# Kernel tuning notes

Measured on AMD Instinct MI355X. Metric: run time of the kernel, lower is better.

The kernel has to match this reference:

```python
import jax, jax.numpy as jnp
import numpy as np

DEPTH_BINS = 39
FEAT = 64
IMG_H, IMG_W = 448, 800
DS = 16
HF, WF = IMG_H // DS, IMG_W // DS  # 28, 50
D_MIN, D_MAX = 2.0, 80.0
BEV_X0 = 0.0
BEV_Y0 = -50.4
RES = 0.8
HB, WB = 188, 126
BN_EPS = 1e-5


def make_frustum():
    # (D, Hf, Wf, 3) points (u*d, v*d, d) at receptive-field centers
    step = (D_MAX - D_MIN) / DEPTH_BINS
    depths = jnp.linspace(D_MIN + step / 2, D_MAX - step / 2, DEPTH_BINS)
    u = jnp.arange(WF, dtype=jnp.float32) * DS + DS / 2
    v = jnp.arange(HF, dtype=jnp.float32) * DS + DS / 2
    d = jnp.broadcast_to(depths[:, None, None], (DEPTH_BINS, HF, WF))
    ug = jnp.broadcast_to(u[None, None, :], (DEPTH_BINS, HF, WF))
    vg = jnp.broadcast_to(v[None, :, None], (DEPTH_BINS, HF, WF))
    return jnp.stack([ug * d, vg * d, d], axis=-1)


def conv2d(x, w, b):
    y = jax.lax.conv_general_dilated(x, w, (1, 1), 'SAME', dimension_numbers=('NCHW', 'OIHW', 'NCHW'))
    return y + b[None, :, None, None]


def bn(x, g, b, m, v):
    s = (g * jax.lax.rsqrt(v + BN_EPS))[None, :, None, None]
    return (x - m[None, :, None, None]) * s + b[None, :, None, None]


def lss_forward(head, intrinsics, car2cams, w1, b1, g1, be1, m1, v1, w2, b2, g2, be2, m2, v2, w3, b3, g3, be3, m3, v3, w4, b4):
    B, N = intrinsics.shape[:2]
    # CamEncoder head: depth softmax x feature outer product (lift)
    depth = jax.nn.softmax(head[:, :DEPTH_BINS], axis=1)       # (BN, D, Hf, Wf)
    feat = head[:, DEPTH_BINS:]                                # (BN, C, Hf, Wf)
    vol = depth[:, :, None] * feat[:, None]                    # (BN, D, C, Hf, Wf)
    vol = vol.reshape(B, N, DEPTH_BINS, FEAT, HF, WF).transpose(0, 1, 2, 4, 5, 3)  # (B,N,D,Hf,Wf,C)
    # get_geometry: frustum -> car frame
    frustum = make_frustum()
    frust_h = jnp.concatenate([frustum, jnp.ones((DEPTH_BINS, HF, WF, 1), jnp.float32)], axis=-1)
    inv_K3 = jnp.linalg.inv(intrinsics)
    inv_K = jnp.zeros((B, N, 4, 4), jnp.float32).at[..., :3, :3].set(inv_K3).at[..., 3, 3].set(1.0)
    T = jnp.linalg.inv(car2cams) @ inv_K                       # (B,N,4,4)
    geom = jnp.einsum('bnij,dhwj->bndhwi', T, frust_h)[..., :3]  # (B,N,D,Hf,Wf,3)
    # voxel_pool: masked scatter-add into BEV grid (int cast truncates toward 0, matching torch .long())
    bx = ((geom[..., 0] - BEV_X0) / RES).astype(jnp.int32)
    by = ((geom[..., 1] - BEV_Y0) / RES).astype(jnp.int32)
    mask = (bx >= 0) & (bx < HB) & (by >= 0) & (by < WB)
    M = N * DEPTH_BINS * HF * WF
    feat_flat = (vol * mask[..., None]).reshape(B * M, FEAT)
    idx = jnp.where(mask, bx * WB + by, 0).reshape(B, M)
    idx = (idx + jnp.arange(B)[:, None] * (HB * WB)).reshape(-1)
    bev = jax.ops.segment_sum(feat_flat, idx, num_segments=B * HB * WB)
    bev = bev.reshape(B, HB, WB, FEAT).transpose(0, 3, 1, 2)   # (B,C,HB,WB)
    # BEVDecoder (eval-mode BN)
    x = jax.nn.relu(bn(conv2d(bev, w1, b1), g1, be1, m1, v1))
    x = jax.nn.relu(bn(conv2d(x, w2, b2), g2, be2, m2, v2))
    x = jax.nn.relu(bn(conv2d(x, w3, b3), g3, be3, m3, v3))
    return conv2d(x, w4, b4)                                   # (B,1,HB,WB)


def setup_inputs() -> dict:
    key = jax.random.key(0)
    ks = jax.random.split(key, 8)
    B, N = 2, 6
    head = jax.random.normal(ks[0], (B * N, DEPTH_BINS + FEAT, HF, WF), dtype=jnp.float32)
    # realistic invertible intrinsics
    f = 500.0 + 25.0 * jax.random.normal(ks[1], (B, N))
    K = (jnp.zeros((B, N, 3, 3))
         .at[..., 0, 0].set(f).at[..., 1, 1].set(f)
         .at[..., 0, 2].set(IMG_W / 2).at[..., 1, 2].set(IMG_H / 2)
         .at[..., 2, 2].set(1.0)).astype(jnp.float32)
    # cam->car rotation: car X = cam z (forward), car Y = -cam x, car Z = -cam y (up)
    R = jnp.array([[0.0, 0.0, 1.0], [-1.0, 0.0, 0.0], [0.0, -1.0, 0.0]], jnp.float32)
    t = jnp.array([2.0, 0.0, 1.3], jnp.float32) + 0.3 * jax.random.normal(ks[2], (B, N, 3))
    cam2car = (jnp.zeros((B, N, 4, 4))
               .at[..., :3, :3].set(R).at[..., :3, 3].set(t).at[..., 3, 3].set(1.0))
    car2cams = jnp.linalg.inv(cam2car).astype(jnp.float32)

    def w(k, shape, fan_in):
        return jax.random.normal(k, shape, dtype=jnp.float32) * (1.0 / np.sqrt(fan_in))

    inp = dict(head=head, intrinsics=K, car2cams=car2cams)
    inp.update(w1=w(ks[3], (128, FEAT, 3, 3), FEAT * 9), b1=jnp.zeros(128), g1=jnp.ones(128), be1=jnp.zeros(128), m1=jnp.zeros(128), v1=jnp.ones(128))
    inp.update(w2=w(ks[4], (128, 128, 3, 3), 128 * 9), b2=jnp.zeros(128), g2=jnp.ones(128), be2=jnp.zeros(128), m2=jnp.zeros(128), v2=jnp.ones(128))
    inp.update(w3=w(ks[5], (64, 128, 3, 3), 128 * 9), b3=jnp.zeros(64), g3=jnp.ones(64), be3=jnp.zeros(64), m3=jnp.zeros(64), v3=jnp.ones(64))
    inp.update(w4=w(ks[6], (1, 64, 1, 1), 64), b4=jnp.zeros(1))
    return inp


def reference(head, intrinsics, car2cams, w1, b1, g1, be1, m1, v1, w2, b2, g2, be2, m2, v2, w3, b3, g3, be3, m3, v3, w4, b4):
    return lss_forward(head, intrinsics, car2cams, w1, b1, g1, be1, m1, v1, w2, b2, g2, be2, m2, v2, w3, b3, g3, be3, m3, v3, w4, b4)
```

## Files before the change

kernel.cpp:

```cpp
#include <hip/hip_runtime.h>
#include <hip/hip_bf16.h>
#include <math.h>

#define NDEPTH 39
#define NFEAT 64
#define HF 28
#define WF 50
#define NPIXCAM (HF*WF)
#define HB 188
#define WB 126
#define NB (HB*WB)
#define BATCH 2
#define NCAM 12
#define NPIX (BATCH*NB)
#define NCELL NPIX
#define CH_IN (NDEPTH+NFEAT)
#define NPT (NCAM*NPIXCAM)
#define NPD (NPT*NDEPTH)
#define CPAD 16
#define SCAN_NB ((NCELL + 255) / 256)

typedef short bf16x8 __attribute__((ext_vector_type(8)));
typedef float f32x4 __attribute__((ext_vector_type(4)));

#define OFF_DIAG 0u
#define OFF_T    64u
#define OFF_B1   1024u
#define OFF_B2   1536u
#define OFF_B3   2048u
#define OFF_WP1  4096u
#define OFF_WP2  151552u
#define OFF_WP3  446464u
#define OFF_XIN  593920u
#define OFF_X1   6658048u
#define OFF_X2   18786304u
#define OFF_PROBS 30914560u
#define OFF_FEATT 33535360u
#define OFF_CUR   35685760u
#define OFF_START 38717824u
#define OFF_BSUM  38907392u
#define OFF_REC   38908416u
#define WS_NEEDED 44150016u

__device__ inline float bfraw2f(unsigned short u) {
  union { unsigned int i; float f; } c; c.i = ((unsigned int)u) << 16; return c.f;
}
__device__ inline float ldf(const void* p, size_t i, int mode) {
  if (mode == 0) return ((const float*)p)[i];
  if (mode == 1) return bfraw2f(((const unsigned short*)p)[i]);
  return (float)(((const _Float16*)p)[i]);
}

__global__ __launch_bounds__(256) void canary_kernel(float* out, int n, float val) {
  int i = blockIdx.x * 256 + threadIdx.x;
  if (i < n) out[i] = val;
}
__global__ __launch_bounds__(256) void probe_kernel(float* out, int n) {
  int i = blockIdx.x * 256 + threadIdx.x;
  if (i < n) out[i] = 16.0f;
}
__global__ void detect_mode_kernel(const void* g1, int* diag) {
  if (threadIdx.x == 0) {
    unsigned int bits = *(const unsigned int*)g1;
    int m = -1;
    if (bits == 0x3F800000u) m = 0;
    else if (bits == 0x3F803F80u) m = 1;
    else if (bits == 0x3C003C00u) m = 2;
    diag[0] = m;
  }
}

__global__ __launch_bounds__(64) void compute_T_kernel(
    const void* __restrict__ K, const void* __restrict__ C,
    const int* __restrict__ diag, float* __restrict__ T) {
  int i = threadIdx.x;
  if (i >= NCAM) return;
  int md = diag[0];
  if (md < 0) return;
  double a = ldf(K, i*9+0, md), b = ldf(K, i*9+1, md), c = ldf(K, i*9+2, md),
         d = ldf(K, i*9+3, md), e = ldf(K, i*9+4, md), f = ldf(K, i*9+5, md),
         g = ldf(K, i*9+6, md), h = ldf(K, i*9+7, md), ii = ldf(K, i*9+8, md);
  double det = a * (e * ii - f * h) - b * (d * ii - f * g) + c * (d * h - e * g);
  double id = 1.0 / det;
  double iK[4][4] = {
      {(e * ii - f * h) * id, (c * h - b * ii) * id, (b * f - c * e) * id, 0.0},
      {(f * g - d * ii) * id, (a * ii - c * g) * id, (c * d - a * f) * id, 0.0},
      {(d * h - e * g) * id, (b * g - a * h) * id, (a * e - b * d) * id, 0.0},
      {0.0, 0.0, 0.0, 1.0}};
  double M[4][8];
  for (int r = 0; r < 4; ++r)
    for (int cc = 0; cc < 4; ++cc) {
      M[r][cc] = ldf(C, (size_t)i * 16 + r * 4 + cc, md);
      M[r][cc + 4] = (r == cc) ? 1.0 : 0.0;
    }
  for (int col = 0; col < 4; ++col) {
    int piv = col;
    double pv = fabs(M[col][col]);
    for (int r = col + 1; r < 4; ++r) {
      double v = fabs(M[r][col]);
      if (v > pv) { pv = v; piv = r; }
    }
    if (piv != col)
      for (int cc = 0; cc < 8; ++cc) {
        double t = M[col][cc]; M[col][cc] = M[piv][cc]; M[piv][cc] = t;
      }
    double inv = 1.0 / M[col][col];
    for (int cc = 0; cc < 8; ++cc) M[col][cc] *= inv;
    for (int r = 0; r < 4; ++r)
      if (r != col) {
        double fa = M[r][col];
        for (int cc = 0; cc < 8; ++cc) M[r][cc] -= fa * M[col][cc];
      }
  }
  for (int r = 0; r < 4; ++r)
    for (int cc = 0; cc < 4; ++cc) {
      double sv = 0.0;
      for (int j = 0; j < 4; ++j) sv += M[r][4 + j] * iK[j][cc];
      T[i * 16 + r * 4 + cc] = (float)sv;
    }
}

__global__ void check_T_kernel(const float* __restrict__ T, int* diag) {
  if (threadIdx.x != 0 || blockIdx.x != 0) return;
  int bad = 0;
  for (int i = 0; i < NCAM * 16; ++i) {
    float x = T[i];
    if (!isfinite(x) || fabsf(x) > 1e7f) bad = 1;
  }
  for (int c = 0; c < NCAM; ++c)
    if (fabsf(T[c * 16 + 15] - 1.0f) > 0.01f) bad = 1;
  if (bad) diag[1] = 1;
}

template <int CIN, int COUT>
__global__ __launch_bounds__(256) void pack_kernel(
    const void* __restrict__ w, const void* __restrict__ bconv,
    const void* __restrict__ g, const void* __restrict__ be,
    const void* __restrict__ m, const void* __restrict__ v,
    const int* __restrict__ diag, __hip_bfloat16* __restrict__ wp,
    float* __restrict__ bias) {
  int md = diag[0];
  if (md < 0) return;
  int t = blockIdx.x * 256 + threadIdx.x;
  if (t < COUT) {
    float s = ldf(g, t, md) * (1.0f / sqrtf(ldf(v, t, md) + 1e-5f));
    bias[t] = (ldf(bconv, t, md) - ldf(m, t, md)) * s + ldf(be, t, md);
  }
  if (t >= 9 * CIN * COUT) return;
  constexpr int NOCB = COUT / 16, NICB = CIN / 32;
  int j = t & 7;
  int l = (t >> 3) & 63;
  int tile = t >> 9;
  int ocb = tile % NOCB;
  int rest = tile / NOCB;
  int icb = rest % NICB;
  int kykx = rest / NICB;
  int ic = icb * 32 + (l >> 4) * 8 + j;
  int oc = ocb * 16 + (l & 15);
  int ky = kykx / 3, kx = kykx - ky * 3;
  float s = ldf(g, oc, md) * (1.0f / sqrtf(ldf(v, oc, md) + 1e-5f));
  float wv = ldf(w, ((size_t)(oc * CIN + ic) * 3 + ky) * 3 + kx, md) * s;
  wp[t] = __float2bfloat16(wv);
}

__device__ inline int point_cell(const float* __restrict__ T, int cam, int rem, int d) {
  int h = rem / WF;
  int w = rem - h * WF;
  const float* Tm = T + cam * 16;
  float u = w * 16.0f + 8.0f;
  float v = h * 16.0f + 8.0f;
  float dep = 3.0f + 2.0f * d;
  float ud = u * dep, vd = v * dep;
  float gx = Tm[0] * ud + Tm[1] * vd + Tm[2] * dep + Tm[3];
  float gy = Tm[4] * ud + Tm[5] * vd + Tm[6] * dep + Tm[7];
  int bx = (int)((gx - 0.0f) / 0.8f);
  int by = (int)((gy - (-50.4f)) / 0.8f);
  if (bx >= 0 && bx < HB && by >= 0 && by < WB) {
    int b = cam / 6;
    return b * NB + bx * WB + by;
  }
  return -1;
}

__global__ __launch_bounds__(64) void prep_kernel2(
    const void* __restrict__ head, const float* __restrict__ T,
    const int* __restrict__ diag, float* __restrict__ probs,
    __hip_bfloat16* __restrict__ featT, int* __restrict__ curpad) {
  int md = diag[0];
  if (md < 0) return;
  int pix = blockIdx.x;
  int cam = pix / NPIXCAM;
  int rem = pix - cam * NPIXCAM;
  int lane = threadIdx.x;
  size_t base = (size_t)cam * CH_IN * NPIXCAM;

  float logit = (lane < NDEPTH) ? ldf(head, base + (size_t)lane * NPIXCAM + rem, md)
                                : -INFINITY;
  float mx = logit;
  for (int o = 32; o; o >>= 1) mx = fmaxf(mx, __shfl_xor(mx, o, 64));
  float e = (lane < NDEPTH) ? expf(logit - mx) : 0.0f;
  float s = e;
  for (int o = 32; o; o >>= 1) s += __shfl_xor(s, o, 64);
  if (lane < NDEPTH) probs[(size_t)pix * NDEPTH + lane] = e / s;

  float feat = ldf(head, base + (size_t)(NDEPTH + lane) * NPIXCAM + rem, md);
  featT[(size_t)pix * NFEAT + lane] = __float2bfloat16(feat);

  if (lane < NDEPTH) {
    int cell = point_cell(T, cam, rem, lane);
    if (cell >= 0) atomicAdd(&curpad[cell * CPAD], 1);
  }
}

__global__ __launch_bounds__(256) void scan_phase1(
    const int* __restrict__ curpad, int* __restrict__ start,
    int* __restrict__ bsum) {
  int cell = blockIdx.x * 256 + threadIdx.x;
  int c = (cell < NCELL) ? curpad[cell * CPAD] : 0;
  __shared__ int sh[256];
  sh[threadIdx.x] = c;
  __syncthreads();
  for (int off = 1; off < 256; off <<= 1) {
    int t = (threadIdx.x >= off) ? sh[threadIdx.x - off] : 0;
    __syncthreads();
    sh[threadIdx.x] += t;
    __syncthreads();
  }
  if (cell < NCELL) start[cell] = sh[threadIdx.x] - c;
  if (threadIdx.x == 255) bsum[blockIdx.x] = sh[255];
}

__global__ __launch_bounds__(256) void scan_phase2(
    int* __restrict__ bsum, int* __restrict__ start) {
  int tid = threadIdx.x;
  int v = (tid < SCAN_NB) ? bsum[tid] : 0;
  __shared__ int sh[256];
  sh[tid] = v;
  __syncthreads();
  for (int off = 1; off < 256; off <<= 1) {
    int t = (tid >= off) ? sh[tid - off] : 0;
    __syncthreads();
    sh[tid] += t;
    __syncthreads();
  }
  if (tid < SCAN_NB) bsum[tid] = sh[tid] - v;
  if (tid == SCAN_NB - 1) start[NCELL] = sh[tid];
}

__global__ __launch_bounds__(256) void scan_phase3(
    int* __restrict__ curpad, int* __restrict__ start,
    const int* __restrict__ bsum) {
  int cell = blockIdx.x * 256 + threadIdx.x;
  if (cell >= NCELL) return;
  int v = start[cell] + bsum[blockIdx.x];
  start[cell] = v;
  curpad[cell * CPAD] = v;
}

__global__ __launch_bounds__(256) void fill_kernel(
    const float* __restrict__ probs, const float* __restrict__ T,
    const int* __restrict__ diag, int* __restrict__ curpad,
    unsigned long long* __restrict__ rec) {
  int md = diag[0];
  if (md < 0) return;
  int tid = blockIdx.x * 256 + threadIdx.x;
  if (tid >= NPD) return;
  int pix = tid / NDEPTH;
  int d = tid - pix * NDEPTH;
  int cam = pix / NPIXCAM;
  int rem = pix - cam * NPIXCAM;
  int cell = point_cell(T, cam, rem, d);
  if (cell < 0) return;
  float p = probs[(size_t)pix * NDEPTH + d];
  int pos = atomicAdd(&curpad[cell * CPAD], 1);
  rec[pos] = ((unsigned long long)__float_as_uint(p) << 32) | (unsigned)pix;
}

__global__ __launch_bounds__(256) void gather_kernel(
    const unsigned long long* __restrict__ rec, const int* __restrict__ start,
    const __hip_bfloat16* __restrict__ featT, __hip_bfloat16* __restrict__ xin) {
  int cell = blockIdx.x;
  int wv = threadIdx.x >> 6;
  int lane = threadIdx.x & 63;
  int s0 = start[cell], s1 = start[cell + 1];
  const unsigned short* ft = (const unsigned short*)featT;
  float acc = 0.0f;
  int j = s0 + wv;
  for (; j + 12 < s1; j += 16) {
    unsigned long long r0 = rec[j];
    unsigned long long r1 = rec[j + 4];
    unsigned long long r2 = rec[j + 8];
    unsigned long long r3 = rec[j + 12];
    float f0 = bfraw2f(ft[(size_t)(unsigned)(r0 & 0xFFFFFFFFull) * NFEAT + lane]);
    float f1 = bfraw2f(ft[(size_t)(unsigned)(r1 & 0xFFFFFFFFull) * NFEAT + lane]);
    float f2 = bfraw2f(ft[(size_t)(unsigned)(r2 & 0xFFFFFFFFull) * NFEAT + lane]);
    float f3 = bfraw2f(ft[(size_t)(unsigned)(r3 & 0xFFFFFFFFull) * NFEAT + lane]);
    acc += __uint_as_float((unsigned)(r0 >> 32)) * f0;
    acc += __uint_as_float((unsigned)(r1 >> 32)) * f1;
    acc += __uint_as_float((unsigned)(r2 >> 32)) * f2;
    acc += __uint_as_float((unsigned)(r3 >> 32)) * f3;
  }
  for (; j < s1; j += 4) {
    unsigned long long r = rec[j];
    acc += __uint_as_float((unsigned)(r >> 32)) *
           bfraw2f(ft[(size_t)(unsigned)(r & 0xFFFFFFFFull) * NFEAT + lane]);
  }
  __shared__ float red[4][64];
  red[wv][lane] = acc;
  __syncthreads();
  if (threadIdx.x < 64) {
    float tot = red[0][lane] + red[1][lane] + red[2][lane] + red[3][lane];
    xin[(size_t)cell * NFEAT + lane] = __float2bfloat16(tot);
  }
}

template <int CIN, int COUT>
__global__ __launch_bounds__(256) void conv_mfma_kernel(
    const __hip_bfloat16* __restrict__ in, const __hip_bfloat16* __restrict__ wp,
    const float* __restrict__ bias, __hip_bfloat16* __restrict__ out) {
  constexpr int NICB = CIN / 32, NOCB = COUT / 16;
  int wv = threadIdx.x >> 6;
  int l = threadIdx.x & 63;
  int pw = blockIdx.x * 64 + wv * 16;
  if (pw >= NPIX) return;
  int m = l & 15;
  int jg = l >> 4;
  int p = pw + m;
  int bq = p / NB;
  int rr = p - bq * NB;
  int y = rr / WB;
  int x = rr - y * WB;

  f32x4 acc[NOCB] = {};

  for (int kykx = 0; kykx < 9; ++kykx) {
    int ky = kykx / 3;
    int dy = ky - 1, dx = kykx - ky * 3 - 1;
    int yy = y + dy, xx = x + dx;
    bool valid = (yy >= 0) & (yy < HB) & (xx >= 0) & (xx < WB);
    int yyc = valid ? yy : 0, xxc = valid ? xx : 0;
    const __hip_bfloat16* arow =
        in + ((size_t)(bq * HB + yyc) * WB + xxc) * CIN + jg * 8;
    const __hip_bfloat16* wpk = wp + (size_t)(kykx * NICB * NOCB) * 512 + l * 8;
#pragma unroll
    for (int icb = 0; icb < NICB; ++icb) {
      bf16x8 a = valid ? *reinterpret_cast<const bf16x8*>(arow + icb * 32)
                       : (bf16x8)(short)0;
#pragma unroll
      for (int ocb = 0; ocb < NOCB; ++ocb) {
        bf16x8 b = *reinterpret_cast<const bf16x8*>(wpk + (icb * NOCB + ocb) * 512);
        acc[ocb] = __builtin_amdgcn_mfma_f32_16x16x32_bf16(a, b, acc[ocb], 0, 0, 0);
      }
    }
  }
#pragma unroll
  for (int ocb = 0; ocb < NOCB; ++ocb) {
    int oc = ocb * 16 + m;
    float bv = bias[oc];
#pragma unroll
    for (int r = 0; r < 4; ++r) {
      int pix = pw + jg * 4 + r;
      float vo = fmaxf(acc[ocb][r] + bv, 0.0f);
      out[(size_t)pix * COUT + oc] = __float2bfloat16(vo);
    }
  }
}

__global__ __launch_bounds__(256) void conv1x1_kernel(
    const __hip_bfloat16* __restrict__ in, const void* __restrict__ w4,
    const void* __restrict__ b4, const int* __restrict__ diag,
    float* __restrict__ out, int npix) {
  int md = diag[0];
  if (md < 0) return;
  int p = blockIdx.x * 256 + threadIdx.x;
  if (p >= npix) return;
  const unsigned short* ip = (const unsigned short*)(in + (size_t)p * NFEAT);
  float acc = 0.0f;
#pragma unroll
  for (int i = 0; i < NFEAT; ++i) acc += bfraw2f(ip[i]) * ldf(w4, i, md);
  out[p] = acc + ldf(b4, 0, md);
}

__global__ __launch_bounds__(256) void final_check_kernel(
    const int* __restrict__ diag, const int* __restrict__ start,
    float* out, int n) {
  float v = 0.0f;
  if (diag[0] < 0) v = 300.0f;
  else if (diag[1]) v = 200.0f;
  else if (start[NCELL] == 0) v = 100.0f;
  if (v == 0.0f) return;
  int i = blockIdx.x * 256 + threadIdx.x;
  if (i < n) out[i] = v;
}

static inline int cdiv(long long a, long long b) { return (int)((a + b - 1) / b); }

extern "C" void kernel_launch(void* const* d_in, const int* in_sizes, int n_in,
                              void* d_out, int out_size, void* d_ws, size_t ws_size,
                              hipStream_t stream) {
  float* out = (float*)d_out;
  size_t out_bytes = (size_t)out_size * sizeof(float);

  hipStreamCaptureStatus cst = hipStreamCaptureStatusNone;
  (void)hipStreamIsCapturing(stream, &cst);
  const bool capturing = (cst != hipStreamCaptureStatusNone);
  hipStream_t s = capturing ? stream : (hipStream_t)0;

#define FINISH()                                                      \
  do {                                                                \
    if (!capturing) {                                                 \
      (void)hipStreamSynchronize(s);                                  \
      (void)hipStreamSynchronize(stream);                             \
      (void)hipDeviceSynchronize();                                   \
    }                                                                 \
  } while (0)

  (void)hipMemsetAsync(d_out, 0x40, out_bytes, s);
  probe_kernel<<<cdiv(out_size, 256), 256, 0, s>>>(out, out_size);

  if (n_in != 23 || in_sizes[0] != NCAM * CH_IN * NPIXCAM) {
    canary_kernel<<<cdiv(out_size, 256), 256, 0, s>>>(out, out_size, 500.0f + n_in);
    FINISH(); return;
  }
  if (in_sizes[1] != NCAM * 9 || in_sizes[2] != NCAM * 16 ||
      in_sizes[3] != 128 * 64 * 9) {
    canary_kernel<<<cdiv(out_size, 256), 256, 0, s>>>(out, out_size, 610.0f);
    FINISH(); return;
  }
  if (out_size != NPIX) {
    canary_kernel<<<cdiv(out_size, 256), 256, 0, s>>>(out, out_size, 700.0f);
    FINISH(); return;
  }
  if (ws_size < WS_NEEDED) {
    canary_kernel<<<cdiv(out_size, 256), 256, 0, s>>>(
        out, out_size, 1000.0f + (float)(ws_size >> 20));
    FINISH(); return;
  }

  const void* head = d_in[0];
  const void* intr = d_in[1];
  const void* c2c  = d_in[2];

  char* ws = (char*)d_ws;
  int*   diag = (int*)(ws + OFF_DIAG);
  float* T    = (float*)(ws + OFF_T);
  float* bb1 = (float*)(ws + OFF_B1);
  float* bb2 = (float*)(ws + OFF_B2);
  float* bb3 = (float*)(ws + OFF_B3);
  __hip_bfloat16* wp1 = (__hip_bfloat16*)(ws + OFF_WP1);
  __hip_bfloat16* wp2 = (__hip_bfloat16*)(ws + OFF_WP2);
  __hip_bfloat16* wp3 = (__hip_bfloat16*)(ws + OFF_WP3);
  __hip_bfloat16* xin = (__hip_bfloat16*)(ws + OFF_XIN);
  __hip_bfloat16* x1  = (__hip_bfloat16*)(ws + OFF_X1);
  __hip_bfloat16* x2  = (__hip_bfloat16*)(ws + OFF_X2);
  __hip_bfloat16* x3  = (__hip_bfloat16*)(ws + OFF_XIN);
  float* probs = (float*)(ws + OFF_PROBS);
  __hip_bfloat16* featT = (__hip_bfloat16*)(ws + OFF_FEATT);
  int* curpad = (int*)(ws + OFF_CUR);
  int* start  = (int*)(ws + OFF_START);
  int* bsum   = (int*)(ws + OFF_BSUM);
  unsigned long long* rec = (unsigned long long*)(ws + OFF_REC);

  (void)hipMemsetAsync(diag, 0, 16, s);
  detect_mode_kernel<<<1, 64, 0, s>>>(d_in[5], diag);
  compute_T_kernel<<<1, 64, 0, s>>>(intr, c2c, diag, T);
  check_T_kernel<<<1, 64, 0, s>>>(T, diag);
  pack_kernel<64, 128><<<288, 256, 0, s>>>(d_in[3], d_in[4], d_in[5], d_in[6],
                                           d_in[7], d_in[8], diag, wp1, bb1);
  pack_kernel<128, 128><<<576, 256, 0, s>>>(d_in[9], d_in[10], d_in[11], d_in[12],
                                            d_in[13], d_in[14], diag, wp2, bb2);
  pack_kernel<128, 64><<<288, 256, 0, s>>>(d_in[15], d_in[16], d_in[17], d_in[18],
                                           d_in[19], d_in[20], diag, wp3, bb3);

  (void)hipMemsetAsync(curpad, 0, (size_t)NCELL * CPAD * 4, s);
  prep_kernel2<<<NPT, 64, 0, s>>>(head, T, diag, probs, featT, curpad);
  scan_phase1<<<SCAN_NB, 256, 0, s>>>(curpad, start, bsum);
  scan_phase2<<<1, 256, 0, s>>>(bsum, start);
  scan_phase3<<<SCAN_NB, 256, 0, s>>>(curpad, start, bsum);
  fill_kernel<<<cdiv(NPD, 256), 256, 0, s>>>(probs, T, diag, curpad, rec);
  gather_kernel<<<NCELL, 256, 0, s>>>(rec, start, featT, xin);

  conv_mfma_kernel<64, 128><<<cdiv(NPIX, 64), 256, 0, s>>>(xin, wp1, bb1, x1);
  conv_mfma_kernel<128, 128><<<cdiv(NPIX, 64), 256, 0, s>>>(x1, wp2, bb2, x2);
  conv_mfma_kernel<128, 64><<<cdiv(NPIX, 64), 256, 0, s>>>(x2, wp3, bb3, x3);
  conv1x1_kernel<<<cdiv(NPIX, 256), 256, 0, s>>>(x3, d_in[21], d_in[22], diag,
                                                 out, NPIX);
  final_check_kernel<<<cdiv(NPIX, 256), 256, 0, s>>>(diag, start, out, NPIX);
  FINISH();
#undef FINISH
}
```

Measured before the change: 308.5 us.

## Compute two pixel tiles per wave in conv MFMA to reuse weight loads

Each wave of the 3x3 conv kernels now processes 32 pixels as two 16-pixel MFMA tiles that share every weight fragment load. This halves weight traffic per output, at the cost of twice the accumulator registers and fewer blocks. Tail pixels are clamped on load and masked on store. Separately, the fill kernel now indexes threads depth-major instead of pixel-major, which changes the order of atomic appends and the probs access pattern.

```diff
diff --git a/kernel.cpp b/kernel.cpp
--- a/kernel.cpp
+++ b/kernel.cpp
@@ -265,8 +265,8 @@
   if (md < 0) return;
   int tid = blockIdx.x * 256 + threadIdx.x;
   if (tid >= NPD) return;
-  int pix = tid / NDEPTH;
-  int d = tid - pix * NDEPTH;
+  int d = tid / NPT;
+  int pix = tid - d * NPT;
   int cam = pix / NPIXCAM;
   int rem = pix - cam * NPIXCAM;
   int cell = point_cell(T, cam, rem, d);
@@ -321,35 +321,50 @@
   constexpr int NICB = CIN / 32, NOCB = COUT / 16;
   int wv = threadIdx.x >> 6;
   int l = threadIdx.x & 63;
-  int pw = blockIdx.x * 64 + wv * 16;
-  if (pw >= NPIX) return;
   int m = l & 15;
   int jg = l >> 4;
-  int p = pw + m;
-  int bq = p / NB;
-  int rr = p - bq * NB;
-  int y = rr / WB;
-  int x = rr - y * WB;
-
-  f32x4 acc[NOCB] = {};
+  int pw = blockIdx.x * 128 + wv * 32;
+  if (pw >= NPIX) return;
+
+  int py[2], px[2], pb[2];
+#pragma unroll
+  for (int t = 0; t < 2; ++t) {
+    int p = pw + t * 16 + m;
+    if (p >= NPIX) p = NPIX - 1;
+    int bq = p / NB;
+    int rr = p - bq * NB;
+    py[t] = rr / WB;
+    px[t] = rr - py[t] * WB;
+    pb[t] = bq;
+  }
+
+  f32x4 acc0[NOCB] = {};
+  f32x4 acc1[NOCB] = {};
 
   for (int kykx = 0; kykx < 9; ++kykx) {
     int ky = kykx / 3;
     int dy = ky - 1, dx = kykx - ky * 3 - 1;
-    int yy = y + dy, xx = x + dx;
-    bool valid = (yy >= 0) & (yy < HB) & (xx >= 0) & (xx < WB);
-    int yyc = valid ? yy : 0, xxc = valid ? xx : 0;
-    const __hip_bfloat16* arow =
-        in + ((size_t)(bq * HB + yyc) * WB + xxc) * CIN + jg * 8;
+    const __hip_bfloat16* arow[2];
+    bool av[2];
+#pragma unroll
+    for (int t = 0; t < 2; ++t) {
+      int yy = py[t] + dy, xx = px[t] + dx;
+      av[t] = (yy >= 0) & (yy < HB) & (xx >= 0) & (xx < WB);
+      int yyc = av[t] ? yy : 0, xxc = av[t] ? xx : 0;
+      arow[t] = in + ((size_t)(pb[t] * HB + yyc) * WB + xxc) * CIN + jg * 8;
+    }
     const __hip_bfloat16* wpk = wp + (size_t)(kykx * NICB * NOCB) * 512 + l * 8;
 #pragma unroll
     for (int icb = 0; icb < NICB; ++icb) {
-      bf16x8 a = valid ? *reinterpret_cast<const bf16x8*>(arow + icb * 32)
-                       : (bf16x8)(short)0;
+      bf16x8 a0 = av[0] ? *reinterpret_cast<const bf16x8*>(arow[0] + icb * 32)
+                        : (bf16x8)(short)0;
+      bf16x8 a1 = av[1] ? *reinterpret_cast<const bf16x8*>(arow[1] + icb * 32)
+                        : (bf16x8)(short)0;
 #pragma unroll
       for (int ocb = 0; ocb < NOCB; ++ocb) {
         bf16x8 b = *reinterpret_cast<const bf16x8*>(wpk + (icb * NOCB + ocb) * 512);
-        acc[ocb] = __builtin_amdgcn_mfma_f32_16x16x32_bf16(a, b, acc[ocb], 0, 0, 0);
+        acc0[ocb] = __builtin_amdgcn_mfma_f32_16x16x32_bf16(a0, b, acc0[ocb], 0, 0, 0);
+        acc1[ocb] = __builtin_amdgcn_mfma_f32_16x16x32_bf16(a1, b, acc1[ocb], 0, 0, 0);
       }
     }
   }
@@ -359,9 +374,16 @@
     float bv = bias[oc];
 #pragma unroll
     for (int r = 0; r < 4; ++r) {
-      int pix = pw + jg * 4 + r;
-      float vo = fmaxf(acc[ocb][r] + bv, 0.0f);
-      out[(size_t)pix * COUT + oc] = __float2bfloat16(vo);
+      int pix0 = pw + jg * 4 + r;
+      if (pix0 < NPIX) {
+        float vo = fmaxf(acc0[ocb][r] + bv, 0.0f);
+        out[(size_t)pix0 * COUT + oc] = __float2bfloat16(vo);
+      }
+      int pix1 = pw + 16 + jg * 4 + r;
+      if (pix1 < NPIX) {
+        float vo = fmaxf(acc1[ocb][r] + bv, 0.0f);
+        out[(size_t)pix1 * COUT + oc] = __float2bfloat16(vo);
+      }
     }
   }
 }
@@ -480,9 +502,9 @@
   fill_kernel<<<cdiv(NPD, 256), 256, 0, s>>>(probs, T, diag, curpad, rec);
   gather_kernel<<<NCELL, 256, 0, s>>>(rec, start, featT, xin);
 
-  conv_mfma_kernel<64, 128><<<cdiv(NPIX, 64), 256, 0, s>>>(xin, wp1, bb1, x1);
-  conv_mfma_kernel<128, 128><<<cdiv(NPIX, 64), 256, 0, s>>>(x1, wp2, bb2, x2);
-  conv_mfma_kernel<128, 64><<<cdiv(NPIX, 64), 256, 0, s>>>(x2, wp3, bb3, x3);
+  conv_mfma_kernel<64, 128><<<cdiv(NPIX, 128), 256, 0, s>>>(xin, wp1, bb1, x1);
+  conv_mfma_kernel<128, 128><<<cdiv(NPIX, 128), 256, 0, s>>>(x1, wp2, bb2, x2);
+  conv_mfma_kernel<128, 64><<<cdiv(NPIX, 128), 256, 0, s>>>(x2, wp3, bb3, x3);
   conv1x1_kernel<<<cdiv(NPIX, 256), 256, 0, s>>>(x3, d_in[21], d_in[22], diag,
                                                  out, NPIX);
   final_check_kernel<<<cdiv(NPIX, 256), 256, 0, s>>>(diag, start, out, NPIX);
```

Result: slower. 340.6 us (+10.4%).
